# Optimization experiments

Hardware: AMD Instinct MI355X
Metric: run time of the kernel (lower is better)

## Reference

```python
import jax, jax.numpy as jnp
import numpy as np

ALPHA = 0.2  # leaky relu slope
NEG_BIG = -9e15


def setup_inputs() -> dict:
    key = jax.random.key(0)
    k1, k2, k3, k4 = jax.random.split(key, 4)
    B, N, Fin, Fout = 8, 2048, 128, 128
    h = jax.random.normal(k1, (B, N, Fin), dtype=jnp.float32)
    adj = jax.random.randint(k2, (N, N), 0, 2, dtype=jnp.int32)
    # xavier_uniform with gain=1.414
    limW = 1.414 * np.sqrt(6.0 / (Fin + Fout))
    W = jax.random.uniform(k3, (Fin, Fout), minval=-limW, maxval=limW, dtype=jnp.float32)
    lima = 1.414 * np.sqrt(6.0 / (2 * Fout + 1))
    a = jax.random.uniform(k4, (2 * Fout, 1), minval=-lima, maxval=lima, dtype=jnp.float32)
    return {"h": h, "adj": adj, "W": W, "a": a}


def reference(h, adj, W, a):
    # Wh: [B, N, F]
    Wh = jnp.einsum("bnf,fo->bno", h, W)
    Fout = W.shape[1]
    a1, a2 = a[:Fout, 0], a[Fout:, 0]  # [F], [F]
    # Additive score decomposition (same math as concat trick):
    # e[b,i,j] = leakyrelu(Wh_i . a1 + Wh_j . a2)
    s1 = Wh @ a1  # [B, N] (source/query part)
    s2 = Wh @ a2  # [B, N] (target part)
    e = s1[:, :, None] + s2[:, None, :]  # [B, N, N]
    e = jnp.where(e > 0, e, ALPHA * e)   # leaky relu
    e = jnp.where(adj[None, :, :] > 0, e, NEG_BIG)
    attention = jax.nn.softmax(e, axis=2)  # [B, N, N]
    # dropout is identity in eval mode
    h_prime = jnp.einsum("bij,bjf->bif", attention, Wh)
    return h_prime
```

## Files before the change

### kernel.cpp

```cpp
#include <hip/hip_runtime.h>
#include <hip/hip_bf16.h>
#include <stdint.h>

#define ALPHA 0.2f

typedef __attribute__((ext_vector_type(8))) short bf16x8;
typedef __attribute__((ext_vector_type(4))) float f32x4;

__device__ __forceinline__ short f2bf(float f) {
    union { float f; uint32_t u; } c; c.f = f;
    uint32_t u = c.u + 0x7FFF + ((c.u >> 16) & 1);
    return (short)(u >> 16);
}

__device__ __forceinline__ uint32_t pk_bf16(float lo, float hi) {
    union { float f; uint32_t u; } a, b;
    a.f = lo; b.f = hi;
    return __builtin_amdgcn_perm(b.u + 0x8000u, a.u + 0x8000u, 0x07060302u);
}

__device__ __forceinline__ void gload_lds16(const void* g, void* l) {
    __builtin_amdgcn_global_load_lds(
        (const __attribute__((address_space(1))) void*)g,
        (__attribute__((address_space(3))) void*)l, 16, 0, 0);
}

__global__ __launch_bounds__(256) void pack_adj_kernel(
        const int* __restrict__ adj, uint8_t* __restrict__ bytes,
        const float* __restrict__ W, short* __restrict__ WTg) {
    int t = blockIdx.x * 256 + threadIdx.x;
    const int4* a4 = reinterpret_cast<const int4*>(adj) + (size_t)t * 2;
    int4 x0 = a4[0], x1 = a4[1];
    uint32_t m = 0;
    m |= (x0.x > 0) ? 1u   : 0u;  m |= (x0.y > 0) ? 2u   : 0u;
    m |= (x0.z > 0) ? 4u   : 0u;  m |= (x0.w > 0) ? 8u   : 0u;
    m |= (x1.x > 0) ? 16u  : 0u;  m |= (x1.y > 0) ? 32u  : 0u;
    m |= (x1.z > 0) ? 64u  : 0u;  m |= (x1.w > 0) ? 128u : 0u;
    bytes[t] = (uint8_t)m;

    if (blockIdx.x < 64) {
        int idx = blockIdx.x * 256 + threadIdx.x;
        int k = idx >> 7, f = idx & 127;
        WTg[f * 128 + k] = f2bf(W[k * 128 + f]);
    }
}

__global__ __launch_bounds__(256) void wh_kernel(
        const float* __restrict__ h, const short* __restrict__ WTg,
        const float* __restrict__ a, short* __restrict__ whT,
        float* __restrict__ s1g, float* __restrict__ s2g) {
    __shared__ float sred[4][2][16];
    __shared__ short tr[4][32][24];

    int tid = threadIdx.x, wid = tid >> 6, lane = tid & 63;
    int q = lane >> 4, n = lane & 15;
    int bb = blockIdx.x & 7;
    int tile = blockIdx.x >> 3;
    int rb = bb * 2048 + tile * 16;
    int row = rb + n;

    f32x4 acc[2] = {};
    #pragma unroll
    for (int kc = 0; kc < 4; ++kc) {
        const float* hp = h + (size_t)row * 128 + kc * 32 + q * 8;
        float4 h0 = reinterpret_cast<const float4*>(hp)[0];
        float4 h1 = reinterpret_cast<const float4*>(hp)[1];
        bf16x8 afrag;
        afrag[0] = f2bf(h0.x); afrag[1] = f2bf(h0.y);
        afrag[2] = f2bf(h0.z); afrag[3] = f2bf(h0.w);
        afrag[4] = f2bf(h1.x); afrag[5] = f2bf(h1.y);
        afrag[6] = f2bf(h1.z); afrag[7] = f2bf(h1.w);
        #pragma unroll
        for (int u = 0; u < 2; ++u) {
            int t = wid * 2 + u;
            bf16x8 bfrag = *reinterpret_cast<const bf16x8*>(
                WTg + (t * 16 + n) * 128 + kc * 32 + q * 8);
            acc[u] = __builtin_amdgcn_mfma_f32_16x16x32_bf16(afrag, bfrag, acc[u], 0, 0, 0);
        }
    }

    float p1[4] = {0.f, 0.f, 0.f, 0.f}, p2[4] = {0.f, 0.f, 0.f, 0.f};
    #pragma unroll
    for (int u = 0; u < 2; ++u) {
        int c = (wid * 2 + u) * 16 + n;
        float a1c = a[c], a2c = a[128 + c];
        #pragma unroll
        for (int r = 0; r < 4; ++r) {
            p1[r] += acc[u][r] * a1c;
            p2[r] += acc[u][r] * a2c;
        }
    }
    #pragma unroll
    for (int d = 1; d < 16; d <<= 1) {
        #pragma unroll
        for (int r = 0; r < 4; ++r) {
            p1[r] += __shfl_xor(p1[r], d);
            p2[r] += __shfl_xor(p2[r], d);
        }
    }
    if (n == 0) {
        #pragma unroll
        for (int r = 0; r < 4; ++r) {
            sred[wid][0][q * 4 + r] = p1[r];
            sred[wid][1][q * 4 + r] = p2[r];
        }
    }

    #pragma unroll
    for (int u = 0; u < 2; ++u)
        #pragma unroll
        for (int r = 0; r < 4; ++r)
            tr[wid][u * 16 + n][q * 4 + r] = f2bf(acc[u][r]);
    __syncthreads();

    if (wid == 0 && lane < 16) {
        float v1 = 0.f, v2 = 0.f;
        #pragma unroll
        for (int v = 0; v < 4; ++v) { v1 += sred[v][0][lane]; v2 += sred[v][1][lane]; }
        s1g[rb + lane] = v1;
        s2g[rb + lane] = v2;
    }

    int jr = rb & 2047;
    int fl = lane & 31, jh = lane >> 5;
    bf16x8 v = *reinterpret_cast<const bf16x8*>(&tr[wid][fl][jh * 8]);
    int f = wid * 32 + fl;
    int t = f >> 4, nn = f & 15;
    int jc = jr >> 5;
    int qg = ((jr & 31) >> 3) + jh;
    *reinterpret_cast<bf16x8*>(
        whT + (size_t)(bb * 64 + jc) * 4096 + t * 512 + qg * 128 + nn * 8) = v;
}

__global__ __launch_bounds__(256) void attn_kernel(
        const short* __restrict__ whT, const float* __restrict__ s1g,
        const float* __restrict__ s2g, const uint8_t* __restrict__ adjb,
        float* __restrict__ out) {
    __shared__ char sbuf[4][8192];
    __shared__ uint32_t mlds[64 * 65];
    __shared__ float s2lds[2048];

    int tid = threadIdx.x, wid = tid >> 6, lane = tid & 63;
    int q = lane >> 4, n = lane & 15;
    int b  = blockIdx.x & 7;
    int ib = (blockIdx.x >> 3) * 64;
    int rowA = ib + wid * 16 + n;

    float s1A = s1g[b * 2048 + rowA];
    const float* s2b = s2g + b * 2048;
    const char* gbase = reinterpret_cast<const char*>(whT) + (size_t)b * 524288;

    {
        int rt = tid >> 2, seg = tid & 3;
        const uint4* src = reinterpret_cast<const uint4*>(
            adjb + (size_t)(ib + rt) * 256 + seg * 64);
        uint32_t* dst = &mlds[rt * 65 + seg * 16];
        #pragma unroll
        for (int i = 0; i < 4; ++i) {
            uint4 v = src[i];
            dst[i * 4 + 0] = v.x; dst[i * 4 + 1] = v.y;
            dst[i * 4 + 2] = v.z; dst[i * 4 + 3] = v.w;
        }
    }
    {
        float4 v0 = *reinterpret_cast<const float4*>(s2b + tid * 8);
        float4 v1 = *reinterpret_cast<const float4*>(s2b + tid * 8 + 4);
        *reinterpret_cast<float4*>(&s2lds[tid * 8])     = v0;
        *reinterpret_cast<float4*>(&s2lds[tid * 8 + 4]) = v1;
    }

    #pragma unroll
    for (int s0 = 0; s0 < 3; ++s0) {
        const char* g = gbase + s0 * 8192 + wid * 2048 + lane * 16;
        char* l = &sbuf[s0][wid * 2048];
        gload_lds16(g, l);
        gload_lds16(g + 1024, l + 1024);
    }
    asm volatile("s_waitcnt vmcnt(4) lgkmcnt(0)" ::: "memory");
    asm volatile("s_barrier" ::: "memory");

    f32x4 acc[8] = {};
    float ds = 0.f;
    int mbase = (wid * 16 + n) * 65;

    for (int s = 0; s < 64; ++s) {
        int sn = (s + 3 <= 63) ? s + 3 : 63;
        {
            const char* g = gbase + (size_t)sn * 8192 + wid * 2048 + lane * 16;
            char* l = &sbuf[(s + 3) & 3][wid * 2048];
            gload_lds16(g, l);
            gload_lds16(g + 1024, l + 1024);
        }

        const char* cb = &sbuf[s & 3][0] + lane * 16;
        bf16x8 nb[8];
        #pragma unroll
        for (int t = 0; t < 8; ++t)
            nb[t] = *reinterpret_cast<const bf16x8*>(cb + t * 1024);

        uint32_t mA = mlds[mbase + s] >> (q * 8);
        float4 s2a = *reinterpret_cast<const float4*>(&s2lds[s * 32 + q * 8]);
        float4 s2c = *reinterpret_cast<const float4*>(&s2lds[s * 32 + q * 8 + 4]);
        float s2arr[8] = {s2a.x, s2a.y, s2a.z, s2a.w,
                          s2c.x, s2c.y, s2c.z, s2c.w};

        float p[8];
        #pragma unroll
        for (int j = 0; j < 8; ++j) {
            float e = s1A + s2arr[j];
            e = fmaxf(e, ALPHA * e);
            float v = ((mA >> j) & 1) ? __expf(e) : 0.0f;
            ds += v; p[j] = v;
        }
        union { uint32_t u32[4]; bf16x8 v; } cv;
        #pragma unroll
        for (int pp = 0; pp < 4; ++pp)
            cv.u32[pp] = pk_bf16(p[2 * pp], p[2 * pp + 1]);

        #pragma unroll
        for (int t = 0; t < 8; ++t)
            acc[t] = __builtin_amdgcn_mfma_f32_16x16x32_bf16(cv.v, nb[t], acc[t], 0, 0, 0);

        asm volatile("s_waitcnt vmcnt(4)" ::: "memory");
        asm volatile("s_barrier" ::: "memory");
    }

    ds += __shfl_xor(ds, 16); ds += __shfl_xor(ds, 32);
    float rd[4];
    #pragma unroll
    for (int r = 0; r < 4; ++r) rd[r] = 1.0f / __shfl(ds, q * 4 + r);

    size_t ob = ((size_t)b * 2048 + ib + wid * 16) * 128;
    #pragma unroll
    for (int t = 0; t < 8; ++t)
        #pragma unroll
        for (int r = 0; r < 4; ++r)
            out[ob + (size_t)(q * 4 + r) * 128 + t * 16 + n] = acc[t][r] * rd[r];
}

extern "C" void kernel_launch(void* const* d_in, const int* in_sizes, int n_in,
                              void* d_out, int out_size, void* d_ws, size_t ws_size,
                              hipStream_t stream) {
    const float* h   = (const float*)d_in[0];
    const int*   adj = (const int*)d_in[1];
    const float* W   = (const float*)d_in[2];
    const float* a   = (const float*)d_in[3];
    float* out = (float*)d_out;

    char* ws = (char*)d_ws;
    short* whT = (short*)ws;
    float* s1  = (float*)(ws + 4194304);
    float* s2  = (float*)(ws + 4259840);
    uint8_t* bytes = (uint8_t*)(ws + 4325376);

    short* WTg = (short*)d_out + (4194304 - 16384);

    pack_adj_kernel<<<2048, 256, 0, stream>>>(adj, bytes, W, WTg);
    wh_kernel<<<1024, 256, 0, stream>>>(h, WTg, a, whT, s1, s2);
    attn_kernel<<<256, 256, 0, stream>>>(whT, s1, s2, bytes, out);
}
```

Measured before the change: 120.2 us.

## Split attention key dimension across wave pairs and double grid size

Each block now handles 32 query rows instead of 64. Its four waves form two row groups times two key halves, and the partial accumulators and softmax denominators are reduced through LDS at the end. The grid doubles to 512 blocks, with launch bounds set to two blocks per CU. The 4-stage ring with counted vmcnt waits is replaced by per-half double buffering with full __syncthreads. The goal is more parallelism across the 256 CUs, since the old grid gave only one block per CU. The cost is an extra LDS reduction and possibly less latency hiding from the shallower pipeline.

```diff
diff --git a/kernel.cpp b/kernel.cpp
--- a/kernel.cpp
+++ b/kernel.cpp
@@ -132,75 +132,76 @@
         whT + (size_t)(bb * 64 + jc) * 4096 + t * 512 + qg * 128 + nn * 8) = v;
 }
 
-__global__ __launch_bounds__(256) void attn_kernel(
+__global__ __launch_bounds__(256, 2) void attn_kernel(
         const short* __restrict__ whT, const float* __restrict__ s1g,
         const float* __restrict__ s2g, const uint8_t* __restrict__ adjb,
         float* __restrict__ out) {
-    __shared__ char sbuf[4][8192];
-    __shared__ uint32_t mlds[64 * 65];
+    __shared__ char ring[2][2][8192];
+    __shared__ uint32_t mlds[32 * 65];
     __shared__ float s2lds[2048];
+    __shared__ float dslds[4][16];
 
     int tid = threadIdx.x, wid = tid >> 6, lane = tid & 63;
     int q = lane >> 4, n = lane & 15;
+    int rg = wid & 1, jh = wid >> 1;
     int b  = blockIdx.x & 7;
-    int ib = (blockIdx.x >> 3) * 64;
-    int rowA = ib + wid * 16 + n;
-
-    float s1A = s1g[b * 2048 + rowA];
-    const float* s2b = s2g + b * 2048;
+    int ib = (blockIdx.x >> 3) * 32;
+    int row = ib + rg * 16 + n;
+
+    float s1A = s1g[b * 2048 + row];
     const char* gbase = reinterpret_cast<const char*>(whT) + (size_t)b * 524288;
 
     {
-        int rt = tid >> 2, seg = tid & 3;
+        int r = tid >> 3, sub = tid & 7;
         const uint4* src = reinterpret_cast<const uint4*>(
-            adjb + (size_t)(ib + rt) * 256 + seg * 64);
-        uint32_t* dst = &mlds[rt * 65 + seg * 16];
-        #pragma unroll
-        for (int i = 0; i < 4; ++i) {
-            uint4 v = src[i];
-            dst[i * 4 + 0] = v.x; dst[i * 4 + 1] = v.y;
-            dst[i * 4 + 2] = v.z; dst[i * 4 + 3] = v.w;
-        }
+            adjb + (size_t)(ib + r) * 256 + sub * 32);
+        uint4 v0 = src[0], v1 = src[1];
+        uint32_t* dst = &mlds[r * 65 + sub * 8];
+        dst[0] = v0.x; dst[1] = v0.y; dst[2] = v0.z; dst[3] = v0.w;
+        dst[4] = v1.x; dst[5] = v1.y; dst[6] = v1.z; dst[7] = v1.w;
     }
     {
+        const float* s2b = s2g + b * 2048;
         float4 v0 = *reinterpret_cast<const float4*>(s2b + tid * 8);
         float4 v1 = *reinterpret_cast<const float4*>(s2b + tid * 8 + 4);
         *reinterpret_cast<float4*>(&s2lds[tid * 8])     = v0;
         *reinterpret_cast<float4*>(&s2lds[tid * 8 + 4]) = v1;
     }
 
-    #pragma unroll
-    for (int s0 = 0; s0 < 3; ++s0) {
-        const char* g = gbase + s0 * 8192 + wid * 2048 + lane * 16;
-        char* l = &sbuf[s0][wid * 2048];
-        gload_lds16(g, l);
-        gload_lds16(g + 1024, l + 1024);
-    }
-    asm volatile("s_waitcnt vmcnt(4) lgkmcnt(0)" ::: "memory");
-    asm volatile("s_barrier" ::: "memory");
+    {
+        const char* g = gbase + (size_t)(jh * 32) * 8192 + rg * 4096 + lane * 16;
+        char* l = &ring[jh][0][rg * 4096];
+        #pragma unroll
+        for (int i = 0; i < 4; ++i)
+            gload_lds16(g + i * 1024, l + i * 1024);
+    }
+    __syncthreads();
 
     f32x4 acc[8] = {};
     float ds = 0.f;
-    int mbase = (wid * 16 + n) * 65;
-
-    for (int s = 0; s < 64; ++s) {
-        int sn = (s + 3 <= 63) ? s + 3 : 63;
-        {
-            const char* g = gbase + (size_t)sn * 8192 + wid * 2048 + lane * 16;
-            char* l = &sbuf[(s + 3) & 3][wid * 2048];
-            gload_lds16(g, l);
-            gload_lds16(g + 1024, l + 1024);
-        }
-
-        const char* cb = &sbuf[s & 3][0] + lane * 16;
+    int mrow = (rg * 16 + n) * 65 + jh * 32;
+
+    for (int c = 0; c < 32; ++c) {
+        int cur = c & 1;
+        if (c < 31) {
+            const char* g = gbase + (size_t)(jh * 32 + c + 1) * 8192
+                            + rg * 4096 + lane * 16;
+            char* l = &ring[jh][cur ^ 1][rg * 4096];
+            #pragma unroll
+            for (int i = 0; i < 4; ++i)
+                gload_lds16(g + i * 1024, l + i * 1024);
+        }
+
+        const char* cb = &ring[jh][cur][0] + lane * 16;
         bf16x8 nb[8];
         #pragma unroll
         for (int t = 0; t < 8; ++t)
             nb[t] = *reinterpret_cast<const bf16x8*>(cb + t * 1024);
 
-        uint32_t mA = mlds[mbase + s] >> (q * 8);
-        float4 s2a = *reinterpret_cast<const float4*>(&s2lds[s * 32 + q * 8]);
-        float4 s2c = *reinterpret_cast<const float4*>(&s2lds[s * 32 + q * 8 + 4]);
+        uint32_t mA = mlds[mrow + c] >> (q * 8);
+        int sb = (jh * 32 + c) * 32 + q * 8;
+        float4 s2a = *reinterpret_cast<const float4*>(&s2lds[sb]);
+        float4 s2c = *reinterpret_cast<const float4*>(&s2lds[sb + 4]);
         float s2arr[8] = {s2a.x, s2a.y, s2a.z, s2a.w,
                           s2c.x, s2c.y, s2c.z, s2c.w};
 
@@ -221,21 +222,38 @@
         for (int t = 0; t < 8; ++t)
             acc[t] = __builtin_amdgcn_mfma_f32_16x16x32_bf16(cv.v, nb[t], acc[t], 0, 0, 0);
 
-        asm volatile("s_waitcnt vmcnt(4)" ::: "memory");
-        asm volatile("s_barrier" ::: "memory");
+        __syncthreads();
     }
 
     ds += __shfl_xor(ds, 16); ds += __shfl_xor(ds, 32);
-    float rd[4];
-    #pragma unroll
-    for (int r = 0; r < 4; ++r) rd[r] = 1.0f / __shfl(ds, q * 4 + r);
-
-    size_t ob = ((size_t)b * 2048 + ib + wid * 16) * 128;
-    #pragma unroll
-    for (int t = 0; t < 8; ++t)
+    if (q == 0) dslds[wid][n] = ds;
+
+    f32x4* cbuf = reinterpret_cast<f32x4*>(&ring[0][0][0]);
+    __syncthreads();
+    if (jh == 1) {
+        #pragma unroll
+        for (int i = 0; i < 8; ++i)
+            cbuf[(rg * 8 + i) * 64 + lane] = acc[i];
+    }
+    __syncthreads();
+    if (jh == 0) {
+        #pragma unroll
+        for (int i = 0; i < 8; ++i)
+            acc[i] += cbuf[(rg * 8 + i) * 64 + lane];
+
+        float dtot = dslds[rg][n] + dslds[2 + rg][n];
+        float rd[4];
         #pragma unroll
         for (int r = 0; r < 4; ++r)
-            out[ob + (size_t)(q * 4 + r) * 128 + t * 16 + n] = acc[t][r] * rd[r];
+            rd[r] = 1.0f / __shfl(dtot, q * 4 + r);
+
+        size_t ob = ((size_t)b * 2048 + ib + rg * 16) * 128;
+        #pragma unroll
+        for (int t = 0; t < 8; ++t)
+            #pragma unroll
+            for (int r = 0; r < 4; ++r)
+                out[ob + (size_t)(q * 4 + r) * 128 + t * 16 + n] = acc[t][r] * rd[r];
+    }
 }
 
 extern "C" void kernel_launch(void* const* d_in, const int* in_sizes, int n_in,
@@ -257,5 +275,5 @@
 
     pack_adj_kernel<<<2048, 256, 0, stream>>>(adj, bytes, W, WTg);
     wh_kernel<<<1024, 256, 0, stream>>>(h, WTg, a, whT, s1, s2);
-    attn_kernel<<<256, 256, 0, stream>>>(whT, s1, s2, bytes, out);
-}
+    attn_kernel<<<512, 256, 0, stream>>>(whT, s1, s2, bytes, out);
+}
```

New measurement: 108.2 us. 1.11x faster.
